# Kernel tuning notes

Measured on AMD Instinct MI355X. Metric: run time of the kernel, lower is better.

The kernel has to match this reference:

```python
import jax, jax.numpy as jnp
import numpy as np

NX = NY = NZ = 128
B = 4
WEIGHT_RESIDU = 1.0
EPS_NEEDLE = 1e-6  # self.epsilon_needle


def lap1d(u, axis):
    """1D Neumann Laplacian (ordre=1) along `axis`: interior [1,-2,1], boundary rows [-1,1]/[1,-1]."""
    u = jnp.moveaxis(u, axis, 0)
    lap = -2.0 * u
    lap = lap.at[:-1].add(u[1:]).at[1:].add(u[:-1])
    # boundary fix: row0 = -u0 + u1, rowN-1 = u_{N-2} - u_{N-1}
    lap = lap.at[0].add(u[0]).at[-1].add(u[-1])
    return jnp.moveaxis(lap, 0, axis)


def setup_inputs() -> dict:
    key = jax.random.key(0)
    k1, k2, k3 = jax.random.split(key, 3)
    output = jax.random.normal(k1, (B, 1, NX, NY, NZ), dtype=jnp.float32)
    gt = jax.random.normal(k2, (B, 1, NX, NY, NZ), dtype=jnp.float32)
    # trinary field in {-1, 0, 1}: g = (input==1), f = (input==-1) + g
    inp = (jax.random.randint(k3, (B, 1, NX, NY, NZ), 0, 3) - 1).astype(jnp.float32)
    return {"output": output, "gt": gt, "input": inp}


def reference(output, gt, input):
    nx, ny, nz = gt.shape[-3], gt.shape[-2], gt.shape[-1]
    dx = 2.0 / (nx - 1)
    dy = 2.0 / (ny - 1)
    dz = 2.0 / (nz - 1)
    a1 = dy / dx
    a2 = dz / dx
    dx2 = dx * dx

    # diagonal of A = -Lap3DNeu (ordre=1): 2 interior / 1 at ends per axis
    def dvec(n):
        return jnp.full((n,), 2.0, dtype=jnp.float32).at[0].set(1.0).at[-1].set(1.0)

    diag_lap = (dvec(nx)[:, None, None]
                + dvec(ny)[None, :, None] / a1**2
                + dvec(nz)[None, None, :] / a2**2)  # (nx,ny,nz)

    # boundary zeroing of b decodes flat index as k*nx*ny + j*nx + i -> (nz,ny,nx) view
    interior = (jnp.zeros((nz, ny, nx), dtype=jnp.float32)
                .at[1:-1, 1:-1, 1:-1].set(1.0).reshape(-1))

    def per_sample(u, img):
        g = (img == 1.0).astype(u.dtype)
        f = (img == -1.0).astype(u.dtype) + g
        f_div_eps = f * (dx2 / EPS_NEEDLE)  # conductivity == 1
        # A_full @ u : 7-point Neumann stencil + needle diagonal
        Au = -(lap1d(u, 0) + lap1d(u, 1) / a1**2 + lap1d(u, 2) / a2**2) + f_div_eps * u
        b = (g * f_div_eps).reshape(-1) * interior
        mx = jnp.max(diag_lap + f_div_eps)  # == torch.max(A_full.to_dense())
        res = jnp.abs(Au.reshape(-1) - b) / mx * (1.0 - f.reshape(-1))
        return WEIGHT_RESIDU * res

    res = jax.vmap(per_sample)(output[:, 0], input[:, 0])  # (B, nx*ny*nz)
    return jnp.mean(res)
```

## Files before the change

### kernel.cpp

```cpp
#include <hip/hip_runtime.h>


namespace {
constexpr int NDIM  = 128;
constexpr int PL    = NDIM * NDIM;
constexpr int NPS   = NDIM * NDIM * NDIM;
constexpr int BATCH = 4;
constexpr int BLOCKS_PER_S = 256;
constexpr int NBLOCKS = BATCH * BLOCKS_PER_S;
}

__device__ __forceinline__ void stencil4(
        const float4& c, const float4& xm, const float4& xp,
        const float4& ym, const float4& yp, float lf_raw, float rg_raw,
        const float4& g, bool klo, bool khi, float dij, const float* dkt,
        float C, float& sum, float& mx) {
    float cc[4] = {c.x, c.y, c.z, c.w};
    float zl[4] = {klo ? c.x : lf_raw, c.x, c.y, c.z};
    float zr[4] = {c.y, c.z, c.w, khi ? c.w : rg_raw};
    float im[4] = {xm.x, xm.y, xm.z, xm.w};
    float ip[4] = {xp.x, xp.y, xp.z, xp.w};
    float jm[4] = {ym.x, ym.y, ym.z, ym.w};
    float jp[4] = {yp.x, yp.y, yp.z, yp.w};
    float gg[4] = {g.x, g.y, g.z, g.w};
#pragma unroll
    for (int t = 0; t < 4; ++t) {
        float lap = (im[t] + ip[t]) + (jm[t] + jp[t]) + (zl[t] + zr[t]) - 6.0f * cc[t];
        bool needle = (gg[t] != 0.0f);
        sum += needle ? 0.0f : fabsf(lap);
        mx = fmaxf(mx, dij + dkt[t] + (needle ? C : 0.0f));
    }
}

__global__ __launch_bounds__(256) void loss_main_k(
        const float* __restrict__ u, const float* __restrict__ img,
        float* __restrict__ psum, float* __restrict__ pmax, float C) {
    int blk = blockIdx.x;
    int b   = blk >> 8;
    int q   = blk & (BLOCKS_PER_S - 1);
    int tid = q * 256 + threadIdx.x;
    int i0  = tid >> 11;
    int j0  = (tid >> 5) & 63;
    int kv  = tid & 31;
    int k4  = kv << 2;

    const float* ub = u   + (size_t)b * NPS;
    const float* gb = img + (size_t)b * NPS;
    int colA = (2 * j0) * NDIM + k4;
    int pbase = 4 * i0;

    int ojm = (j0 == 0)  ? 0 : -NDIM;
    int ojp = (j0 == 63) ? 0 :  NDIM;
    float djA = (j0 == 0)  ? 1.0f : 2.0f;
    float djB = (j0 == 63) ? 1.0f : 2.0f;
    float dkt[4] = { (kv == 0) ? 1.0f : 2.0f, 2.0f, 2.0f,
                     (kv == 31) ? 1.0f : 2.0f };
    bool klo = (kv == 0), khi = (kv == 31);

    float4 cA[6], cB[6];
#pragma unroll
    for (int w = 0; w < 6; ++w) {
        int p = pbase - 1 + w;
        p = (p < 0) ? 0 : (p > NDIM - 1 ? NDIM - 1 : p);
        const float* pa = ub + p * PL + colA;
        cA[w] = *(const float4*)pa;
        cB[w] = *(const float4*)(pa + NDIM);
    }
    float4 ymA[4], ypB[4], gA[4], gB[4];
#pragma unroll
    for (int s = 0; s < 4; ++s) {
        const float* pa = ub + (pbase + s) * PL + colA;
        ymA[s] = *(const float4*)(pa + ojm);
        ypB[s] = *(const float4*)(pa + NDIM + ojp);
        const float* pg = gb + (pbase + s) * PL + colA;
        gA[s] = *(const float4*)pg;
        gB[s] = *(const float4*)(pg + NDIM);
    }

    float sum = 0.0f, mx = 0.0f;
#pragma unroll
    for (int s = 0; s < 4; ++s) {
        float di = 2.0f;
        if (i0 == 0  && s == 0) di = 1.0f;
        if (i0 == 31 && s == 3) di = 1.0f;
        float lfA = __shfl_up(cA[s + 1].w, 1), rgA = __shfl_down(cA[s + 1].x, 1);
        float lfB = __shfl_up(cB[s + 1].w, 1), rgB = __shfl_down(cB[s + 1].x, 1);
        stencil4(cA[s + 1], cA[s], cA[s + 2], ymA[s], cB[s + 1], lfA, rgA,
                 gA[s], klo, khi, di + djA, dkt, C, sum, mx);
        stencil4(cB[s + 1], cB[s], cB[s + 2], cA[s + 1], ypB[s], lfB, rgB,
                 gB[s], klo, khi, di + djB, dkt, C, sum, mx);
    }

#pragma unroll
    for (int off = 32; off > 0; off >>= 1) {
        sum += __shfl_down(sum, off);
        mx = fmaxf(mx, __shfl_down(mx, off));
    }
    __shared__ float ssum[4], smax[4];
    int wave = threadIdx.x >> 6, lane = threadIdx.x & 63;
    if (lane == 0) { ssum[wave] = sum; smax[wave] = mx; }
    __syncthreads();
    if (threadIdx.x == 0) {
        psum[blk] = (ssum[0] + ssum[1]) + (ssum[2] + ssum[3]);
        pmax[blk] = fmaxf(fmaxf(smax[0], smax[1]), fmaxf(smax[2], smax[3]));
    }
}

__global__ __launch_bounds__(256) void finalize_k(const float* __restrict__ psum,
                                                  const float* __restrict__ pmax,
                                                  float* __restrict__ out) {
    int wave = threadIdx.x >> 6, lane = threadIdx.x & 63;
    double s = 0.0; float m = 0.0f;
    int base = wave * BLOCKS_PER_S;
#pragma unroll
    for (int r = 0; r < BLOCKS_PER_S / 64; ++r) {
        int idx = base + r * 64 + lane;
        s += (double)psum[idx];
        m = fmaxf(m, pmax[idx]);
    }
#pragma unroll
    for (int off = 32; off > 0; off >>= 1) {
        s += __shfl_down(s, off);
        m = fmaxf(m, __shfl_down(m, off));
    }
    __shared__ double ws[4]; __shared__ float wm[4];
    if (lane == 0) { ws[wave] = s; wm[wave] = m; }
    __syncthreads();
    if (threadIdx.x == 0) {
        double tot = 0.0;
        for (int b = 0; b < BATCH; ++b) tot += ws[b] / (double)wm[b];
        out[0] = (float)(tot / ((double)BATCH * (double)NPS));
    }
}

extern "C" void kernel_launch(void* const* d_in, const int* in_sizes, int n_in,
                              void* d_out, int out_size, void* d_ws, size_t ws_size,
                              hipStream_t stream) {
    const float* u   = (const float*)d_in[0];
    const float* img = (const float*)d_in[2];
    float* out = (float*)d_out;

    float* psum = (float*)d_ws;
    float* pmax = psum + NBLOCKS;

    const double dx = 2.0 / (NDIM - 1);
    const float  C  = (float)((dx * dx) / 1e-6);

    hipLaunchKernelGGL(loss_main_k, dim3(NBLOCKS), dim3(256), 0, stream,
                       u, img, psum, pmax, C);
    hipLaunchKernelGGL(finalize_k, dim3(1), dim3(256), 0, stream, psum, pmax, out);
}
```

Measured before the change: 19.40 us.

## Shrink per-thread work to one i-plane and quadruple block count

Each thread now handles a single x-plane (two j-rows of 4 k-values) instead of four consecutive planes, so there are four times as many blocks and far fewer registers per thread, with launch bounds requesting 8 blocks per CU. The intent is higher occupancy and more parallelism to hide memory latency. The cost is less reuse along x: each plane's neighbours are loaded separately, so the central rows are read about three times and global traffic grows. The finalize kernel has to reduce four times as many partials.

```diff
diff --git a/kernel.cpp b/kernel.cpp
--- a/kernel.cpp
+++ b/kernel.cpp
@@ -6,7 +6,7 @@
 constexpr int PL    = NDIM * NDIM;
 constexpr int NPS   = NDIM * NDIM * NDIM;
 constexpr int BATCH = 4;
-constexpr int BLOCKS_PER_S = 256;
+constexpr int BLOCKS_PER_S = 1024;
 constexpr int NBLOCKS = BATCH * BLOCKS_PER_S;
 }
 
@@ -32,64 +32,51 @@
     }
 }
 
-__global__ __launch_bounds__(256) void loss_main_k(
+__global__ __launch_bounds__(256, 8) void loss_main_k(
         const float* __restrict__ u, const float* __restrict__ img,
         float* __restrict__ psum, float* __restrict__ pmax, float C) {
     int blk = blockIdx.x;
-    int b   = blk >> 8;
+    int b   = blk >> 10;
     int q   = blk & (BLOCKS_PER_S - 1);
-    int tid = q * 256 + threadIdx.x;
-    int i0  = tid >> 11;
-    int j0  = (tid >> 5) & 63;
-    int kv  = tid & 31;
+    int t   = threadIdx.x;
+    int i   = q >> 3;
+    int j0  = (q & 7) * 8 + ((t >> 5) & 7);
+    int kv  = t & 31;
     int k4  = kv << 2;
 
     const float* ub = u   + (size_t)b * NPS;
     const float* gb = img + (size_t)b * NPS;
-    int colA = (2 * j0) * NDIM + k4;
-    int pbase = 4 * i0;
+    int rowA = (i * NDIM + 2 * j0) * NDIM + k4;
 
     int ojm = (j0 == 0)  ? 0 : -NDIM;
     int ojp = (j0 == 63) ? 0 :  NDIM;
+    int oim = (i == 0)          ? 0 : -PL;
+    int oip = (i == NDIM - 1)   ? 0 :  PL;
+    float di  = (i == 0 || i == NDIM - 1) ? 1.0f : 2.0f;
     float djA = (j0 == 0)  ? 1.0f : 2.0f;
     float djB = (j0 == 63) ? 1.0f : 2.0f;
     float dkt[4] = { (kv == 0) ? 1.0f : 2.0f, 2.0f, 2.0f,
                      (kv == 31) ? 1.0f : 2.0f };
     bool klo = (kv == 0), khi = (kv == 31);
 
-    float4 cA[6], cB[6];
-#pragma unroll
-    for (int w = 0; w < 6; ++w) {
-        int p = pbase - 1 + w;
-        p = (p < 0) ? 0 : (p > NDIM - 1 ? NDIM - 1 : p);
-        const float* pa = ub + p * PL + colA;
-        cA[w] = *(const float4*)pa;
-        cB[w] = *(const float4*)(pa + NDIM);
-    }
-    float4 ymA[4], ypB[4], gA[4], gB[4];
-#pragma unroll
-    for (int s = 0; s < 4; ++s) {
-        const float* pa = ub + (pbase + s) * PL + colA;
-        ymA[s] = *(const float4*)(pa + ojm);
-        ypB[s] = *(const float4*)(pa + NDIM + ojp);
-        const float* pg = gb + (pbase + s) * PL + colA;
-        gA[s] = *(const float4*)pg;
-        gB[s] = *(const float4*)(pg + NDIM);
-    }
+    const float* pa = ub + rowA;
+    float4 cA  = *(const float4*)pa;
+    float4 cB  = *(const float4*)(pa + NDIM);
+    float4 ymA = *(const float4*)(pa + ojm);
+    float4 ypB = *(const float4*)(pa + NDIM + ojp);
+    float4 xmA = *(const float4*)(pa + oim);
+    float4 xmB = *(const float4*)(pa + oim + NDIM);
+    float4 xpA = *(const float4*)(pa + oip);
+    float4 xpB = *(const float4*)(pa + oip + NDIM);
+    const float* pg = gb + rowA;
+    float4 gA  = *(const float4*)pg;
+    float4 gB  = *(const float4*)(pg + NDIM);
 
     float sum = 0.0f, mx = 0.0f;
-#pragma unroll
-    for (int s = 0; s < 4; ++s) {
-        float di = 2.0f;
-        if (i0 == 0  && s == 0) di = 1.0f;
-        if (i0 == 31 && s == 3) di = 1.0f;
-        float lfA = __shfl_up(cA[s + 1].w, 1), rgA = __shfl_down(cA[s + 1].x, 1);
-        float lfB = __shfl_up(cB[s + 1].w, 1), rgB = __shfl_down(cB[s + 1].x, 1);
-        stencil4(cA[s + 1], cA[s], cA[s + 2], ymA[s], cB[s + 1], lfA, rgA,
-                 gA[s], klo, khi, di + djA, dkt, C, sum, mx);
-        stencil4(cB[s + 1], cB[s], cB[s + 2], cA[s + 1], ypB[s], lfB, rgB,
-                 gB[s], klo, khi, di + djB, dkt, C, sum, mx);
-    }
+    float lfA = __shfl_up(cA.w, 1), rgA = __shfl_down(cA.x, 1);
+    float lfB = __shfl_up(cB.w, 1), rgB = __shfl_down(cB.x, 1);
+    stencil4(cA, xmA, xpA, ymA, cB, lfA, rgA, gA, klo, khi, di + djA, dkt, C, sum, mx);
+    stencil4(cB, xmB, xpB, cA, ypB, lfB, rgB, gB, klo, khi, di + djB, dkt, C, sum, mx);
 
 #pragma unroll
     for (int off = 32; off > 0; off >>= 1) {
```

Result: faster. 18.41 us (-5.1%).
